# Kernel tuning notes

Hardware: AMD Instinct MI355X
Metric: run time of the kernel (lower is better)

Reference implementation:

```python
import jax, jax.numpy as jnp
import numpy as np

B, V, D = 8, 2048, 3
CL1_F, CL1_K = 64, 6
CL2_F, CL2_K = 128, 5
F1, F2 = 512, 256


def _uniform(k, shape, fin, fout):
    s = np.sqrt(2.0 / (fin + fout)).astype(np.float32)
    return jax.random.uniform(k, shape, jnp.float32, -s, s)


def setup_inputs() -> dict:
    key = jax.random.key(0)
    ks = jax.random.split(key, 8)
    x = jax.random.normal(ks[0], (B, D, V), jnp.float32)
    # dense stand-in for the scaled graph Laplacian; scaled so spectral radius < 1
    L = jax.random.normal(ks[1], (B, V, V), jnp.float32) * (0.5 / np.sqrt(V))
    L = 0.5 * (L + L.transpose(0, 2, 1))  # symmetric like a real Laplacian
    return {
        "x": x,
        "L": L,
        "cl1_w": _uniform(ks[2], (CL1_F, D * CL1_K), CL1_K, CL1_F),
        "cl1_b": jnp.zeros((CL1_F,), jnp.float32),
        "cl2_w": _uniform(ks[3], (CL2_F, CL2_K * CL1_F), CL2_K * CL1_F, CL2_F),
        "cl2_b": jnp.zeros((CL2_F,), jnp.float32),
        "fc1_w": _uniform(ks[4], (F1, CL2_F), CL2_F, F1),
        "fc1_b": jnp.zeros((F1,), jnp.float32),
        "fc2_w": _uniform(ks[5], (F2, F1), F1, F2),
        "fc2_b": jnp.zeros((F2,), jnp.float32),
    }


def _cheby_conv(x, L, W, b, K):
    # x: [B, V, Fin], L: [B, V, V] -> [B, V, Fout]
    x0 = x
    xs = [x0]
    if K > 1:
        x1 = jnp.einsum('bvu,buf->bvf', L, x0)
        xs.append(x1)
    for _ in range(2, K):
        x2 = 2.0 * jnp.einsum('bvu,buf->bvf', L, x1) - x0
        xs.append(x2)
        x0, x1 = x1, x2
    # torch ordering: feature index = fin * K + k  -> stack K on last axis
    xk = jnp.stack(xs, axis=-1)                 # [B, V, Fin, K]
    xk = xk.reshape(xk.shape[0], xk.shape[1], -1)  # [B, V, Fin*K]
    return xk @ W.T + b


def reference(x, L, cl1_w, cl1_b, cl2_w, cl2_b, fc1_w, fc1_b, fc2_w, fc2_b):
    xp = x.transpose(0, 2, 1)                    # [B, V, D]
    y = jax.nn.relu(_cheby_conv(xp, L, cl1_w, cl1_b, CL1_K))
    y = jax.nn.relu(_cheby_conv(y, L, cl2_w, cl2_b, CL2_K))
    y = jax.nn.relu(y @ fc1_w.T + fc1_b)
    y = jax.nn.relu(y @ fc2_w.T + fc2_b)
    return y                                     # [B, V, F2]
```

## Files before the change

### kernel.cpp

```cpp
#include <hip/hip_runtime.h>

#define B_ 8
#define V_ 2048
#define D_ 3
#define M_ (B_*V_)

typedef __attribute__((ext_vector_type(8))) short short8;
typedef __attribute__((ext_vector_type(4))) float f32x4;

__device__ inline void async_copy16(const void* g, void* lds) {
  __builtin_amdgcn_global_load_lds(
      (const __attribute__((address_space(1))) unsigned int*)g,
      (__attribute__((address_space(3))) unsigned int*)lds, 16, 0, 0);
}

__device__ inline void split_bf16(float v, short& hi, short& lo) {
  unsigned u  = __float_as_uint(v);
  unsigned hb = u & 0xFFFF0000u;
  float d = v - __uint_as_float(hb);
  hi = (short)(hb >> 16);
  lo = (short)(__float_as_uint(d) >> 16);
}

__global__ __launch_bounds__(256) void k_zero(float4* __restrict__ p, int n4) {
  int i = blockIdx.x * 256 + threadIdx.x;
  if (i < n4) p[i] = float4{0.f, 0.f, 0.f, 0.f};
}

__global__ __launch_bounds__(256) void k_split_pad(const float* __restrict__ src,
    short* __restrict__ dh, short* __restrict__ dl, int N, int K, int Kpad) {
  int idx = blockIdx.x * 256 + threadIdx.x;
  if (idx >= N * Kpad) return;
  int n = idx / Kpad, k = idx - n * Kpad;
  float v = (k < K) ? src[(size_t)n*K + k] : 0.f;
  short hi, lo; split_bf16(v, hi, lo);
  dh[idx] = hi; dl[idx] = lo;
}

__global__ __launch_bounds__(256) void k_transpose(const float* __restrict__ x,
    float* __restrict__ x0, short* __restrict__ XKh, short* __restrict__ XKl) {
  int i = blockIdx.x * 256 + threadIdx.x;
  if (i >= B_*V_*D_) return;
  int f = i % D_;
  int v = (i / D_) % V_;
  int b = i / (D_*V_);
  float val = x[((size_t)b*D_ + f)*V_ + v];
  x0[i] = val;
  short hi, lo; split_bf16(val, hi, lo);
  size_t o = ((size_t)b*V_ + v)*64 + f*6;
  XKh[o] = hi; XKl[o] = lo;
}

__global__ __launch_bounds__(256) void k_cheby1(const float* __restrict__ L,
    const float* __restrict__ xc, const float* __restrict__ xp,
    float* __restrict__ xn, short* __restrict__ XKh, short* __restrict__ XKl,
    float alpha, float beta, int kidx) {
  __shared__ float sx[3][V_];
  int b  = blockIdx.x >> 6;
  int r0 = (blockIdx.x & 63) * 32;
  const float* xcb = xc + (size_t)b*V_*D_;
  for (int i = threadIdx.x; i < V_*D_; i += 256) {
    int u = i / 3, f = i - u*3;
    sx[f][u] = xcb[i];
  }
  __syncthreads();
  int w = threadIdx.x >> 6, lane = threadIdx.x & 63;
  const float4* X0 = (const float4*)sx[0];
  const float4* X1 = (const float4*)sx[1];
  const float4* X2 = (const float4*)sx[2];
  for (int pass = 0; pass < 4; pass++) {
    int rA = r0 + pass*8 + w*2;
    int rB = rA + 1;
    const float4* LA = (const float4*)(L + ((size_t)b*V_ + rA)*V_);
    const float4* LB = (const float4*)(L + ((size_t)b*V_ + rB)*V_);
    float a0=0.f,a1=0.f,a2=0.f,b0=0.f,b1=0.f,b2=0.f;
    #pragma unroll
    for (int it = 0; it < 8; it++) {
      int u4 = it*64 + lane;
      float4 la = LA[u4], lb = LB[u4];
      float4 x0 = X0[u4], x1 = X1[u4], x2 = X2[u4];
      a0 = fmaf(la.x,x0.x,fmaf(la.y,x0.y,fmaf(la.z,x0.z,fmaf(la.w,x0.w,a0))));
      a1 = fmaf(la.x,x1.x,fmaf(la.y,x1.y,fmaf(la.z,x1.z,fmaf(la.w,x1.w,a1))));
      a2 = fmaf(la.x,x2.x,fmaf(la.y,x2.y,fmaf(la.z,x2.z,fmaf(la.w,x2.w,a2))));
      b0 = fmaf(lb.x,x0.x,fmaf(lb.y,x0.y,fmaf(lb.z,x0.z,fmaf(lb.w,x0.w,b0))));
      b1 = fmaf(lb.x,x1.x,fmaf(lb.y,x1.y,fmaf(lb.z,x1.z,fmaf(lb.w,x1.w,b1))));
      b2 = fmaf(lb.x,x2.x,fmaf(lb.y,x2.y,fmaf(lb.z,x2.z,fmaf(lb.w,x2.w,b2))));
    }
    #pragma unroll
    for (int off = 32; off > 0; off >>= 1) {
      a0 += __shfl_down(a0, off); a1 += __shfl_down(a1, off);
      a2 += __shfl_down(a2, off); b0 += __shfl_down(b0, off);
      b1 += __shfl_down(b1, off); b2 += __shfl_down(b2, off);
    }
    if (lane == 0) {
      float vA[3] = {alpha*a0, alpha*a1, alpha*a2};
      float vB[3] = {alpha*b0, alpha*b1, alpha*b2};
      size_t baseA = ((size_t)b*V_ + rA)*3;
      size_t baseB = ((size_t)b*V_ + rB)*3;
      if (beta != 0.f) {
        #pragma unroll
        for (int f = 0; f < 3; f++) {
          vA[f] -= beta * xp[baseA + f];
          vB[f] -= beta * xp[baseB + f];
        }
      }
      #pragma unroll
      for (int f = 0; f < 3; f++) {
        xn[baseA + f] = vA[f];
        xn[baseB + f] = vB[f];
        short hi, lo;
        split_bf16(vA[f], hi, lo);
        size_t oA = ((size_t)b*V_ + rA)*64 + f*6 + kidx;
        XKh[oA] = hi; XKl[oA] = lo;
        split_bf16(vB[f], hi, lo);
        size_t oB = ((size_t)b*V_ + rB)*64 + f*6 + kidx;
        XKh[oB] = hi; XKl[oB] = lo;
      }
    }
  }
}

__global__ __launch_bounds__(256) void k_split_t(const float* __restrict__ Z,
    short* __restrict__ Th, short* __restrict__ Tl) {
  __shared__ float t[64][65];
  int b  = blockIdx.x >> 5;
  int r0 = (blockIdx.x & 31) * 64;
  const float* Zb = Z + ((size_t)b*V_ + r0)*64;
  #pragma unroll 4
  for (int i = 0; i < 16; i++) {
    int idx = i*256 + threadIdx.x;
    int r = idx >> 6, n = idx & 63;
    t[r][n] = Zb[(size_t)r*64 + n];
  }
  __syncthreads();
  #pragma unroll 4
  for (int i = 0; i < 16; i++) {
    int idx = i*256 + threadIdx.x;
    int n = idx >> 6, r = idx & 63;
    short hi, lo; split_bf16(t[r][n], hi, lo);
    size_t o = ((size_t)b*64 + n)*V_ + r0 + r;
    Th[o] = hi; Tl[o] = lo;
  }
}

__global__ __launch_bounds__(256) void k_cheby2_mfma(const float* __restrict__ L,
    const short* __restrict__ Zth, const short* __restrict__ Ztl,
    const float* __restrict__ Zp,
    float* __restrict__ Zn, short* __restrict__ ZKh, short* __restrict__ ZKl,
    short* __restrict__ Znth, short* __restrict__ Zntl,
    float alpha, float beta, int kidx) {
  __shared__ float sA[32*64];
  __shared__ short sBh[64*64];
  __shared__ short sBl[64*64];

  int b  = blockIdx.x >> 6;
  int r0 = (blockIdx.x & 63) * 32;
  const float* Lb   = L   + (size_t)b*V_*V_;
  const short* Zthb = Zth + (size_t)b*64*V_;
  const short* Ztlb = Ztl + (size_t)b*64*V_;

  int tid  = threadIdx.x;
  int w    = tid >> 6;
  int lane = tid & 63;
  int lm   = lane & 15;
  int quad = lane >> 4;
  int h     = (w & 1) * 16;
  int cbase = (w >> 1) * 32;

  const f32x4*  sAv  = (const f32x4*)sA;
  const short8* sBhv = (const short8*)sBh;
  const short8* sBlv = (const short8*)sBl;

  f32x4 acc0 = {0.f,0.f,0.f,0.f};
  f32x4 acc1 = {0.f,0.f,0.f,0.f};

  for (int s = 0; s < V_/64; s++) {
    int k0 = s * 64;
    if (s) __syncthreads();
    #pragma unroll
    for (int t = 0; t < 2; t++) {
      int f = t*256 + tid;
      int r = f >> 4, cc = f & 15;
      int c = cc ^ (r & 15);
      async_copy16(Lb + (size_t)(r0 + r)*V_ + k0 + c*4, &sA[f*4]);
    }
    #pragma unroll
    for (int t = 0; t < 2; t++) {
      int f = t*256 + tid;
      int n = f >> 3, cc = f & 7;
      int c = cc ^ (n & 7);
      async_copy16(Zthb + (size_t)n*V_ + k0 + c*8, &sBh[f*8]);
      async_copy16(Ztlb + (size_t)n*V_ + k0 + c*8, &sBl[f*8]);
    }
    __syncthreads();

    #pragma unroll
    for (int ks = 0; ks < 2; ks++) {
      int koff = ks * 32;
      int r = h + lm;
      int c0 = (koff >> 2) + 2*quad;
      f32x4 a0 = sAv[r*16 + (c0 ^ (r & 15))];
      f32x4 a1 = sAv[r*16 + ((c0 + 1) ^ (r & 15))];
      float av[8] = {a0.x, a0.y, a0.z, a0.w, a1.x, a1.y, a1.z, a1.w};
      short8 ah, al;
      #pragma unroll
      for (int j = 0; j < 8; j++) {
        short hi, lo; split_bf16(av[j], hi, lo);
        ah[j] = hi; al[j] = lo;
      }
      int cb = (koff >> 3) + quad;
      {
        int n = cbase + lm;
        short8 bh = sBhv[n*8 + (cb ^ (n & 7))];
        short8 bl = sBlv[n*8 + (cb ^ (n & 7))];
        acc0 = __builtin_amdgcn_mfma_f32_16x16x32_bf16(ah, bh, acc0, 0, 0, 0);
        acc0 = __builtin_amdgcn_mfma_f32_16x16x32_bf16(ah, bl, acc0, 0, 0, 0);
        acc0 = __builtin_amdgcn_mfma_f32_16x16x32_bf16(al, bh, acc0, 0, 0, 0);
      }
      {
        int n = cbase + 16 + lm;
        short8 bh = sBhv[n*8 + (cb ^ (n & 7))];
        short8 bl = sBlv[n*8 + (cb ^ (n & 7))];
        acc1 = __builtin_amdgcn_mfma_f32_16x16x32_bf16(ah, bh, acc1, 0, 0, 0);
        acc1 = __builtin_amdgcn_mfma_f32_16x16x32_bf16(ah, bl, acc1, 0, 0, 0);
        acc1 = __builtin_amdgcn_mfma_f32_16x16x32_bf16(al, bh, acc1, 0, 0, 0);
      }
    }
  }

  #pragma unroll
  for (int ct = 0; ct < 2; ct++) {
    f32x4 a = ct ? acc1 : acc0;
    int n = cbase + ct*16 + lm;
    #pragma unroll
    for (int i = 0; i < 4; i++) {
      int r = r0 + h + quad*4 + i;
      size_t rowb = (size_t)b*V_ + r;
      float v = alpha * a[i];
      if (beta != 0.f) v -= beta * Zp[rowb*64 + n];
      Zn[rowb*64 + n] = v;
      short hi, lo; split_bf16(v, hi, lo);
      size_t ok = rowb*320 + (size_t)n*5 + kidx;
      ZKh[ok] = hi; ZKl[ok] = lo;
      size_t o = ((size_t)b*64 + n)*V_ + r;
      Znth[o] = hi; Zntl[o] = lo;
    }
  }
}

__global__ __launch_bounds__(256) void k_gemm_bf16(
    const short* __restrict__ Ah, const short* __restrict__ Al,
    const short* __restrict__ Wh, const short* __restrict__ Wl,
    const float* __restrict__ bias, int N, int K,
    float* __restrict__ Cf, short* __restrict__ Ch, short* __restrict__ Cl,
    short* __restrict__ Ph, short* __restrict__ Pl,
    int packMul, int packStride) {
  __shared__ short sAh[64*64], sAl[64*64], sWh[64*64], sWl[64*64];
  int bm = blockIdx.x & 255;
  int bn = blockIdx.x >> 8;
  int row0 = bm * 64, col0 = bn * 64;
  int tid = threadIdx.x, w = tid >> 6, lane = tid & 63;
  int lm = lane & 15, quad = lane >> 4;
  int wm = (w & 1) * 32, wn = (w >> 1) * 32;

  const short8* vAh = (const short8*)sAh;
  const short8* vAl = (const short8*)sAl;
  const short8* vWh = (const short8*)sWh;
  const short8* vWl = (const short8*)sWl;

  f32x4 acc[2][2] = {{{0.f,0.f,0.f,0.f},{0.f,0.f,0.f,0.f}},
                     {{0.f,0.f,0.f,0.f},{0.f,0.f,0.f,0.f}}};

  for (int k0 = 0; k0 < K; k0 += 64) {
    if (k0) __syncthreads();
    #pragma unroll
    for (int t = 0; t < 2; t++) {
      int f = t*256 + tid;
      int r = f >> 3, p = f & 7;
      int c = p ^ (r & 7);
      size_t goA = (size_t)(row0 + r)*K + k0 + c*8;
      size_t goW = (size_t)(col0 + r)*K + k0 + c*8;
      async_copy16(Ah + goA, &sAh[f*8]);
      async_copy16(Al + goA, &sAl[f*8]);
      async_copy16(Wh + goW, &sWh[f*8]);
      async_copy16(Wl + goW, &sWl[f*8]);
    }
    __syncthreads();

    #pragma unroll
    for (int ks = 0; ks < 2; ks++) {
      int kc = ks*4 + quad;
      short8 a_h[2], a_l[2], b_h[2], b_l[2];
      #pragma unroll
      for (int i = 0; i < 2; i++) {
        int m = wm + i*16 + lm;
        a_h[i] = vAh[m*8 + (kc ^ (m & 7))];
        a_l[i] = vAl[m*8 + (kc ^ (m & 7))];
      }
      #pragma unroll
      for (int j = 0; j < 2; j++) {
        int n = wn + j*16 + lm;
        b_h[j] = vWh[n*8 + (kc ^ (n & 7))];
        b_l[j] = vWl[n*8 + (kc ^ (n & 7))];
      }
      #pragma unroll
      for (int i = 0; i < 2; i++)
        #pragma unroll
        for (int j = 0; j < 2; j++) {
          acc[i][j] = __builtin_amdgcn_mfma_f32_16x16x32_bf16(a_h[i], b_h[j], acc[i][j], 0, 0, 0);
          acc[i][j] = __builtin_amdgcn_mfma_f32_16x16x32_bf16(a_h[i], b_l[j], acc[i][j], 0, 0, 0);
          acc[i][j] = __builtin_amdgcn_mfma_f32_16x16x32_bf16(a_l[i], b_h[j], acc[i][j], 0, 0, 0);
        }
    }
  }

  #pragma unroll
  for (int i = 0; i < 2; i++)
    #pragma unroll
    for (int j = 0; j < 2; j++) {
      int col = col0 + wn + j*16 + lm;
      float bj = bias[col];
      #pragma unroll
      for (int g = 0; g < 4; g++) {
        int row = row0 + wm + i*16 + quad*4 + g;
        float v = acc[i][j][g] + bj;
        v = v > 0.f ? v : 0.f;
        if (Cf) Cf[(size_t)row*N + col] = v;
        if (Ch) {
          short hi, lo; split_bf16(v, hi, lo);
          Ch[(size_t)row*N + col] = hi;
          Cl[(size_t)row*N + col] = lo;
        }
        if (Ph) {
          short hi, lo; split_bf16(v, hi, lo);
          size_t o = (size_t)row*packStride + (size_t)col*packMul;
          Ph[o] = hi; Pl[o] = lo;
        }
      }
    }
}

extern "C" void kernel_launch(void* const* d_in, const int* in_sizes, int n_in,
                              void* d_out, int out_size, void* d_ws, size_t ws_size,
                              hipStream_t stream) {
  const float* x   = (const float*)d_in[0];
  const float* L   = (const float*)d_in[1];
  const float* w1  = (const float*)d_in[2];
  const float* b1  = (const float*)d_in[3];
  const float* w2  = (const float*)d_in[4];
  const float* b2  = (const float*)d_in[5];
  const float* fw1 = (const float*)d_in[6];
  const float* fb1 = (const float*)d_in[7];
  const float* fw2 = (const float*)d_in[8];
  const float* fb2 = (const float*)d_in[9];
  float* out = (float*)d_out;

  float* p  = (float*)d_ws;
  float* xa = p;  p += (size_t)B_*V_*D_;
  float* xb = p;  p += (size_t)B_*V_*D_;
  float* xc = p;  p += (size_t)B_*V_*D_;
  float* y1 = p;  p += (size_t)M_*64;
  float* zb = p;  p += (size_t)M_*64;
  float* zc = p;  p += (size_t)M_*64;
  short* sp = (short*)p;
  short* ZKh = sp;  sp += (size_t)M_*320;
  short* ZKl = sp;  sp += (size_t)M_*320;
  short* y2h = sp;  sp += (size_t)M_*128;
  short* y2l = sp;  sp += (size_t)M_*128;
  short* h1h = sp;  sp += (size_t)M_*512;
  short* h1l = sp;  sp += (size_t)M_*512;
  short* ZtAh = sp; sp += (size_t)M_*64;
  short* ZtAl = sp; sp += (size_t)M_*64;
  short* ZtBh = sp; sp += (size_t)M_*64;
  short* ZtBl = sp; sp += (size_t)M_*64;
  short* w1h = sp;  sp += 64*64;
  short* w1l = sp;  sp += 64*64;
  short* w2h = sp;  sp += 128*320;
  short* w2l = sp;  sp += 128*320;
  short* fw1h = sp; sp += 512*128;
  short* fw1l = sp; sp += 512*128;
  short* fw2h = sp; sp += 256*512;
  short* fw2l = sp; sp += 256*512;
  short* XKh = h1h;
  short* XKl = h1h + (size_t)M_*64;

  dim3 blk(256);

  k_zero<<<1024, blk, 0, stream>>>((float4*)XKh, (M_*128) / 8);

  k_split_pad<<<(64*64+255)/256,   blk, 0, stream>>>(w1,  w1h,  w1l,  64, 18, 64);
  k_split_pad<<<(128*320+255)/256, blk, 0, stream>>>(w2,  w2h,  w2l,  128, 320, 320);
  k_split_pad<<<(512*128+255)/256, blk, 0, stream>>>(fw1, fw1h, fw1l, 512, 128, 128);
  k_split_pad<<<(256*512+255)/256, blk, 0, stream>>>(fw2, fw2h, fw2l, 256, 512, 512);

  k_transpose<<<(B_*V_*D_ + 255)/256, blk, 0, stream>>>(x, xa, XKh, XKl);

  k_cheby1<<<512, blk, 0, stream>>>(L, xa, xa, xb, XKh, XKl, 1.f, 0.f, 1);
  k_cheby1<<<512, blk, 0, stream>>>(L, xb, xa, xc, XKh, XKl, 2.f, 1.f, 2);
  k_cheby1<<<512, blk, 0, stream>>>(L, xc, xb, xa, XKh, XKl, 2.f, 1.f, 3);
  k_cheby1<<<512, blk, 0, stream>>>(L, xa, xc, xb, XKh, XKl, 2.f, 1.f, 4);
  k_cheby1<<<512, blk, 0, stream>>>(L, xb, xa, xc, XKh, XKl, 2.f, 1.f, 5);

  k_gemm_bf16<<<256, blk, 0, stream>>>(XKh, XKl, w1h, w1l, b1, 64, 64,
                                       y1, nullptr, nullptr, ZKh, ZKl, 5, 320);

  k_split_t<<<256, blk, 0, stream>>>(y1, ZtAh, ZtAl);

  k_cheby2_mfma<<<512, blk, 0, stream>>>(L, ZtAh, ZtAl, y1, zb, ZKh, ZKl,
                                         ZtBh, ZtBl, 1.f, 0.f, 1);
  k_cheby2_mfma<<<512, blk, 0, stream>>>(L, ZtBh, ZtBl, y1, zc, ZKh, ZKl,
                                         ZtAh, ZtAl, 2.f, 1.f, 2);
  k_cheby2_mfma<<<512, blk, 0, stream>>>(L, ZtAh, ZtAl, zb, y1, ZKh, ZKl,
                                         ZtBh, ZtBl, 2.f, 1.f, 3);
  k_cheby2_mfma<<<512, blk, 0, stream>>>(L, ZtBh, ZtBl, zc, zb, ZKh, ZKl,
                                         ZtAh, ZtAl, 2.f, 1.f, 4);

  k_gemm_bf16<<<512, blk, 0, stream>>>(ZKh, ZKl, w2h, w2l, b2, 128, 320,
                                       nullptr, y2h, y2l, nullptr, nullptr, 0, 0);
  k_gemm_bf16<<<2048, blk, 0, stream>>>(y2h, y2l, fw1h, fw1l, fb1, 512, 128,
                                        nullptr, h1h, h1l, nullptr, nullptr, 0, 0);
  k_gemm_bf16<<<1024, blk, 0, stream>>>(h1h, h1l, fw2h, fw2l, fb2, 256, 512,
                                        out, nullptr, nullptr, nullptr, nullptr, 0, 0);
}
```

Measured before the change: 594.7 us.

## Fuse prep kernels, shrink Chebyshev row tiles, fold transpose into first GEMM

Merges the zero-fill, weight split/pad and input transpose launches into one prep kernel. It also fuses the y1 transpose-split into the first GEMM epilogue, which drops the separate k_split_t pass. The Chebyshev kernels now use smaller row tiles (8 rows for cheby1, 16 for cheby2), which quadruples or doubles the grid to spread the L-bandwidth-bound work over more CUs. In exchange, each block reloads the x/Z operand more often: cheby1 restages all of x into LDS per block, and more blocks now read the full Zt slices.

New measurement: 540.1 us. 9.2% less time.

```diff
diff --git a/kernel.cpp b/kernel.cpp
--- a/kernel.cpp
+++ b/kernel.cpp
@@ -22,33 +22,43 @@
   lo = (short)(__float_as_uint(d) >> 16);
 }
 
-__global__ __launch_bounds__(256) void k_zero(float4* __restrict__ p, int n4) {
+__global__ __launch_bounds__(256) void k_prep(
+    const float* __restrict__ x,
+    const float* __restrict__ w1, const float* __restrict__ w2,
+    const float* __restrict__ fw1, const float* __restrict__ fw2,
+    float* __restrict__ xa,
+    short* __restrict__ XKh, short* __restrict__ XKl,
+    short* __restrict__ w1h, short* __restrict__ w1l,
+    short* __restrict__ w2h, short* __restrict__ w2l,
+    short* __restrict__ fw1h, short* __restrict__ fw1l,
+    short* __restrict__ fw2h, short* __restrict__ fw2l) {
   int i = blockIdx.x * 256 + threadIdx.x;
-  if (i < n4) p[i] = float4{0.f, 0.f, 0.f, 0.f};
-}
-
-__global__ __launch_bounds__(256) void k_split_pad(const float* __restrict__ src,
-    short* __restrict__ dh, short* __restrict__ dl, int N, int K, int Kpad) {
-  int idx = blockIdx.x * 256 + threadIdx.x;
-  if (idx >= N * Kpad) return;
-  int n = idx / Kpad, k = idx - n * Kpad;
-  float v = (k < K) ? src[(size_t)n*K + k] : 0.f;
-  short hi, lo; split_bf16(v, hi, lo);
-  dh[idx] = hi; dl[idx] = lo;
-}
-
-__global__ __launch_bounds__(256) void k_transpose(const float* __restrict__ x,
-    float* __restrict__ x0, short* __restrict__ XKh, short* __restrict__ XKl) {
-  int i = blockIdx.x * 256 + threadIdx.x;
-  if (i >= B_*V_*D_) return;
-  int f = i % D_;
-  int v = (i / D_) % V_;
-  int b = i / (D_*V_);
-  float val = x[((size_t)b*D_ + f)*V_ + v];
-  x0[i] = val;
-  short hi, lo; split_bf16(val, hi, lo);
-  size_t o = ((size_t)b*V_ + v)*64 + f*6;
-  XKh[o] = hi; XKl[o] = lo;
+  short hi, lo;
+  if (i < M_*64) {
+    int r = i >> 6, s = i & 63;
+    float val = 0.f;
+    if (s == 0 || s == 6 || s == 12) {
+      int f = s / 6;
+      int b = r >> 11, v = r & (V_-1);
+      val = x[((size_t)b*D_ + f)*V_ + v];
+      xa[(size_t)r*3 + f] = val;
+    }
+    split_bf16(val, hi, lo);
+    XKh[i] = hi; XKl[i] = lo;
+    return;
+  }
+  i -= M_*64;
+  if (i < 4096) {
+    int n = i >> 6, k = i & 63;
+    float v = (k < 18) ? w1[n*18 + k] : 0.f;
+    split_bf16(v, hi, lo); w1h[i] = hi; w1l[i] = lo; return;
+  }
+  i -= 4096;
+  if (i < 40960) { split_bf16(w2[i],  hi, lo); w2h[i]=hi;  w2l[i]=lo;  return; }
+  i -= 40960;
+  if (i < 65536) { split_bf16(fw1[i], hi, lo); fw1h[i]=hi; fw1l[i]=lo; return; }
+  i -= 65536;
+  if (i < 131072){ split_bf16(fw2[i], hi, lo); fw2h[i]=hi; fw2l[i]=lo; return; }
 }
 
 __global__ __launch_bounds__(256) void k_cheby1(const float* __restrict__ L,
@@ -56,8 +66,8 @@
     float* __restrict__ xn, short* __restrict__ XKh, short* __restrict__ XKl,
     float alpha, float beta, int kidx) {
   __shared__ float sx[3][V_];
-  int b  = blockIdx.x >> 6;
-  int r0 = (blockIdx.x & 63) * 32;
+  int b  = blockIdx.x >> 8;
+  int r0 = (blockIdx.x & 255) * 8;
   const float* xcb = xc + (size_t)b*V_*D_;
   for (int i = threadIdx.x; i < V_*D_; i += 256) {
     int u = i / 3, f = i - u*3;
@@ -68,78 +78,53 @@
   const float4* X0 = (const float4*)sx[0];
   const float4* X1 = (const float4*)sx[1];
   const float4* X2 = (const float4*)sx[2];
-  for (int pass = 0; pass < 4; pass++) {
-    int rA = r0 + pass*8 + w*2;
-    int rB = rA + 1;
-    const float4* LA = (const float4*)(L + ((size_t)b*V_ + rA)*V_);
-    const float4* LB = (const float4*)(L + ((size_t)b*V_ + rB)*V_);
-    float a0=0.f,a1=0.f,a2=0.f,b0=0.f,b1=0.f,b2=0.f;
-    #pragma unroll
-    for (int it = 0; it < 8; it++) {
-      int u4 = it*64 + lane;
-      float4 la = LA[u4], lb = LB[u4];
-      float4 x0 = X0[u4], x1 = X1[u4], x2 = X2[u4];
-      a0 = fmaf(la.x,x0.x,fmaf(la.y,x0.y,fmaf(la.z,x0.z,fmaf(la.w,x0.w,a0))));
-      a1 = fmaf(la.x,x1.x,fmaf(la.y,x1.y,fmaf(la.z,x1.z,fmaf(la.w,x1.w,a1))));
-      a2 = fmaf(la.x,x2.x,fmaf(la.y,x2.y,fmaf(la.z,x2.z,fmaf(la.w,x2.w,a2))));
-      b0 = fmaf(lb.x,x0.x,fmaf(lb.y,x0.y,fmaf(lb.z,x0.z,fmaf(lb.w,x0.w,b0))));
-      b1 = fmaf(lb.x,x1.x,fmaf(lb.y,x1.y,fmaf(lb.z,x1.z,fmaf(lb.w,x1.w,b1))));
-      b2 = fmaf(lb.x,x2.x,fmaf(lb.y,x2.y,fmaf(lb.z,x2.z,fmaf(lb.w,x2.w,b2))));
-    }
-    #pragma unroll
-    for (int off = 32; off > 0; off >>= 1) {
-      a0 += __shfl_down(a0, off); a1 += __shfl_down(a1, off);
-      a2 += __shfl_down(a2, off); b0 += __shfl_down(b0, off);
-      b1 += __shfl_down(b1, off); b2 += __shfl_down(b2, off);
-    }
-    if (lane == 0) {
-      float vA[3] = {alpha*a0, alpha*a1, alpha*a2};
-      float vB[3] = {alpha*b0, alpha*b1, alpha*b2};
-      size_t baseA = ((size_t)b*V_ + rA)*3;
-      size_t baseB = ((size_t)b*V_ + rB)*3;
-      if (beta != 0.f) {
-        #pragma unroll
-        for (int f = 0; f < 3; f++) {
-          vA[f] -= beta * xp[baseA + f];
-          vB[f] -= beta * xp[baseB + f];
-        }
+  int rA = r0 + w*2;
+  int rB = rA + 1;
+  const float4* LA = (const float4*)(L + ((size_t)b*V_ + rA)*V_);
+  const float4* LB = (const float4*)(L + ((size_t)b*V_ + rB)*V_);
+  float a0=0.f,a1=0.f,a2=0.f,b0=0.f,b1=0.f,b2=0.f;
+  #pragma unroll
+  for (int it = 0; it < 8; it++) {
+    int u4 = it*64 + lane;
+    float4 la = LA[u4], lb = LB[u4];
+    float4 x0 = X0[u4], x1 = X1[u4], x2 = X2[u4];
+    a0 = fmaf(la.x,x0.x,fmaf(la.y,x0.y,fmaf(la.z,x0.z,fmaf(la.w,x0.w,a0))));
+    a1 = fmaf(la.x,x1.x,fmaf(la.y,x1.y,fmaf(la.z,x1.z,fmaf(la.w,x1.w,a1))));
+    a2 = fmaf(la.x,x2.x,fmaf(la.y,x2.y,fmaf(la.z,x2.z,fmaf(la.w,x2.w,a2))));
+    b0 = fmaf(lb.x,x0.x,fmaf(lb.y,x0.y,fmaf(lb.z,x0.z,fmaf(lb.w,x0.w,b0))));
+    b1 = fmaf(lb.x,x1.x,fmaf(lb.y,x1.y,fmaf(lb.z,x1.z,fmaf(lb.w,x1.w,b1))));
+    b2 = fmaf(lb.x,x2.x,fmaf(lb.y,x2.y,fmaf(lb.z,x2.z,fmaf(lb.w,x2.w,b2))));
+  }
+  #pragma unroll
+  for (int off = 32; off > 0; off >>= 1) {
+    a0 += __shfl_down(a0, off); a1 += __shfl_down(a1, off);
+    a2 += __shfl_down(a2, off); b0 += __shfl_down(b0, off);
+    b1 += __shfl_down(b1, off); b2 += __shfl_down(b2, off);
+  }
+  if (lane == 0) {
+    float vA[3] = {alpha*a0, alpha*a1, alpha*a2};
+    float vB[3] = {alpha*b0, alpha*b1, alpha*b2};
+    size_t baseA = ((size_t)b*V_ + rA)*3;
+    size_t baseB = ((size_t)b*V_ + rB)*3;
+    if (beta != 0.f) {
+      #pragma unroll
+      for (int f = 0; f < 3; f++) {
+        vA[f] -= beta * xp[baseA + f];
+        vB[f] -= beta * xp[baseB + f];
       }
-      #pragma unroll
-      for (int f = 0; f < 3; f++) {
-        xn[baseA + f] = vA[f];
-        xn[baseB + f] = vB[f];
-        short hi, lo;
-        split_bf16(vA[f], hi, lo);
-        size_t oA = ((size_t)b*V_ + rA)*64 + f*6 + kidx;
-        XKh[oA] = hi; XKl[oA] = lo;
-        split_bf16(vB[f], hi, lo);
-        size_t oB = ((size_t)b*V_ + rB)*64 + f*6 + kidx;
-        XKh[oB] = hi; XKl[oB] = lo;
-      }
-    }
-  }
-}
-
-__global__ __launch_bounds__(256) void k_split_t(const float* __restrict__ Z,
-    short* __restrict__ Th, short* __restrict__ Tl) {
-  __shared__ float t[64][65];
-  int b  = blockIdx.x >> 5;
-  int r0 = (blockIdx.x & 31) * 64;
-  const float* Zb = Z + ((size_t)b*V_ + r0)*64;
-  #pragma unroll 4
-  for (int i = 0; i < 16; i++) {
-    int idx = i*256 + threadIdx.x;
-    int r = idx >> 6, n = idx & 63;
-    t[r][n] = Zb[(size_t)r*64 + n];
-  }
-  __syncthreads();
-  #pragma unroll 4
-  for (int i = 0; i < 16; i++) {
-    int idx = i*256 + threadIdx.x;
-    int n = idx >> 6, r = idx & 63;
-    short hi, lo; split_bf16(t[r][n], hi, lo);
-    size_t o = ((size_t)b*64 + n)*V_ + r0 + r;
-    Th[o] = hi; Tl[o] = lo;
+    }
+    #pragma unroll
+    for (int f = 0; f < 3; f++) {
+      xn[baseA + f] = vA[f];
+      xn[baseB + f] = vB[f];
+      short hi, lo;
+      split_bf16(vA[f], hi, lo);
+      size_t oA = ((size_t)b*V_ + rA)*64 + f*6 + kidx;
+      XKh[oA] = hi; XKl[oA] = lo;
+      split_bf16(vB[f], hi, lo);
+      size_t oB = ((size_t)b*V_ + rB)*64 + f*6 + kidx;
+      XKh[oB] = hi; XKl[oB] = lo;
+    }
   }
 }
 
@@ -149,12 +134,12 @@
     float* __restrict__ Zn, short* __restrict__ ZKh, short* __restrict__ ZKl,
     short* __restrict__ Znth, short* __restrict__ Zntl,
     float alpha, float beta, int kidx) {
-  __shared__ float sA[32*64];
+  __shared__ float sA[16*64];
   __shared__ short sBh[64*64];
   __shared__ short sBl[64*64];
 
-  int b  = blockIdx.x >> 6;
-  int r0 = (blockIdx.x & 63) * 32;
+  int b  = blockIdx.x >> 7;
+  int r0 = (blockIdx.x & 127) * 16;
   const float* Lb   = L   + (size_t)b*V_*V_;
   const short* Zthb = Zth + (size_t)b*64*V_;
   const short* Ztlb = Ztl + (size_t)b*64*V_;
@@ -164,24 +149,21 @@
   int lane = tid & 63;
   int lm   = lane & 15;
   int quad = lane >> 4;
-  int h     = (w & 1) * 16;
-  int cbase = (w >> 1) * 32;
+  int cbase = w * 16;
 
   const f32x4*  sAv  = (const f32x4*)sA;
   const short8* sBhv = (const short8*)sBh;
   const short8* sBlv = (const short8*)sBl;
 
-  f32x4 acc0 = {0.f,0.f,0.f,0.f};
-  f32x4 acc1 = {0.f,0.f,0.f,0.f};
+  f32x4 acc = {0.f,0.f,0.f,0.f};
 
   for (int s = 0; s < V_/64; s++) {
     int k0 = s * 64;
     if (s) __syncthreads();
-    #pragma unroll
-    for (int t = 0; t < 2; t++) {
-      int f = t*256 + tid;
+    {
+      int f = tid;
       int r = f >> 4, cc = f & 15;
-      int c = cc ^ (r & 15);
+      int c = cc ^ r;
       async_copy16(Lb + (size_t)(r0 + r)*V_ + k0 + c*4, &sA[f*4]);
     }
     #pragma unroll
@@ -197,10 +179,10 @@
     #pragma unroll
     for (int ks = 0; ks < 2; ks++) {
       int koff = ks * 32;
-      int r = h + lm;
+      int r = lm;
       int c0 = (koff >> 2) + 2*quad;
-      f32x4 a0 = sAv[r*16 + (c0 ^ (r & 15))];
-      f32x4 a1 = sAv[r*16 + ((c0 + 1) ^ (r & 15))];
+      f32x4 a0 = sAv[r*16 + (c0 ^ r)];
+      f32x4 a1 = sAv[r*16 + ((c0 + 1) ^ r)];
       float av[8] = {a0.x, a0.y, a0.z, a0.w, a1.x, a1.y, a1.z, a1.w};
       short8 ah, al;
       #pragma unroll
@@ -209,56 +191,39 @@
         ah[j] = hi; al[j] = lo;
       }
       int cb = (koff >> 3) + quad;
-      {
-        int n = cbase + lm;
-        short8 bh = sBhv[n*8 + (cb ^ (n & 7))];
-        short8 bl = sBlv[n*8 + (cb ^ (n & 7))];
-        acc0 = __builtin_amdgcn_mfma_f32_16x16x32_bf16(ah, bh, acc0, 0, 0, 0);
-        acc0 = __builtin_amdgcn_mfma_f32_16x16x32_bf16(ah, bl, acc0, 0, 0, 0);
-        acc0 = __builtin_amdgcn_mfma_f32_16x16x32_bf16(al, bh, acc0, 0, 0, 0);
-      }
-      {
-        int n = cbase + 16 + lm;
-        short8 bh = sBhv[n*8 + (cb ^ (n & 7))];
-        short8 bl = sBlv[n*8 + (cb ^ (n & 7))];
-        acc1 = __builtin_amdgcn_mfma_f32_16x16x32_bf16(ah, bh, acc1, 0, 0, 0);
-        acc1 = __builtin_amdgcn_mfma_f32_16x16x32_bf16(ah, bl, acc1, 0, 0, 0);
-        acc1 = __builtin_amdgcn_mfma_f32_16x16x32_bf16(al, bh, acc1, 0, 0, 0);
-      }
-    }
-  }
-
+      int n = cbase + lm;
+      short8 bh = sBhv[n*8 + (cb ^ (n & 7))];
+      short8 bl = sBlv[n*8 + (cb ^ (n & 7))];
+      acc = __builtin_amdgcn_mfma_f32_16x16x32_bf16(ah, bh, acc, 0, 0, 0);
+      acc = __builtin_amdgcn_mfma_f32_16x16x32_bf16(ah, bl, acc, 0, 0, 0);
+      acc = __builtin_amdgcn_mfma_f32_16x16x32_bf16(al, bh, acc, 0, 0, 0);
+    }
+  }
+
+  int n = cbase + lm;
   #pragma unroll
-  for (int ct = 0; ct < 2; ct++) {
-    f32x4 a = ct ? acc1 : acc0;
-    int n = cbase + ct*16 + lm;
-    #pragma unroll
-    for (int i = 0; i < 4; i++) {
-      int r = r0 + h + quad*4 + i;
-      size_t rowb = (size_t)b*V_ + r;
-      float v = alpha * a[i];
-      if (beta != 0.f) v -= beta * Zp[rowb*64 + n];
-      Zn[rowb*64 + n] = v;
-      short hi, lo; split_bf16(v, hi, lo);
-      size_t ok = rowb*320 + (size_t)n*5 + kidx;
-      ZKh[ok] = hi; ZKl[ok] = lo;
-      size_t o = ((size_t)b*64 + n)*V_ + r;
-      Znth[o] = hi; Zntl[o] = lo;
-    }
-  }
-}
-
-__global__ __launch_bounds__(256) void k_gemm_bf16(
+  for (int i = 0; i < 4; i++) {
+    int r = r0 + quad*4 + i;
+    size_t rowb = (size_t)b*V_ + r;
+    float v = alpha * acc[i];
+    if (beta != 0.f) v -= beta * Zp[rowb*64 + n];
+    Zn[rowb*64 + n] = v;
+    short hi, lo; split_bf16(v, hi, lo);
+    size_t ok = rowb*320 + (size_t)n*5 + kidx;
+    ZKh[ok] = hi; ZKl[ok] = lo;
+    size_t o = ((size_t)b*64 + n)*V_ + r;
+    Znth[o] = hi; Zntl[o] = lo;
+  }
+}
+
+__device__ __forceinline__ void gemm_tile(
     const short* __restrict__ Ah, const short* __restrict__ Al,
     const short* __restrict__ Wh, const short* __restrict__ Wl,
-    const float* __restrict__ bias, int N, int K,
+    const float* __restrict__ bias, int N, int K, int row0, int col0,
+    short* sAh, short* sAl, short* sWh, short* sWl,
     float* __restrict__ Cf, short* __restrict__ Ch, short* __restrict__ Cl,
-    short* __restrict__ Ph, short* __restrict__ Pl,
-    int packMul, int packStride) {
-  __shared__ short sAh[64*64], sAl[64*64], sWh[64*64], sWl[64*64];
-  int bm = blockIdx.x & 255;
-  int bn = blockIdx.x >> 8;
-  int row0 = bm * 64, col0 = bn * 64;
+    short* __restrict__ Ph, short* __restrict__ Pl, int packMul, int packStride,
+    short* __restrict__ Th, short* __restrict__ Tl) {
   int tid = threadIdx.x, w = tid >> 6, lane = tid & 63;
   int lm = lane & 15, quad = lane >> 4;
   int wm = (w & 1) * 32, wn = (w >> 1) * 32;
@@ -326,18 +291,48 @@
         float v = acc[i][j][g] + bj;
         v = v > 0.f ? v : 0.f;
         if (Cf) Cf[(size_t)row*N + col] = v;
+        short hi, lo;
+        if (Ch || Ph || Th) split_bf16(v, hi, lo);
         if (Ch) {
-          short hi, lo; split_bf16(v, hi, lo);
           Ch[(size_t)row*N + col] = hi;
           Cl[(size_t)row*N + col] = lo;
         }
         if (Ph) {
-          short hi, lo; split_bf16(v, hi, lo);
           size_t o = (size_t)row*packStride + (size_t)col*packMul;
           Ph[o] = hi; Pl[o] = lo;
         }
+        if (Th) {
+          int bb = row >> 11, vv = row & (V_-1);
+          size_t o = ((size_t)bb*64 + col)*V_ + vv;
+          Th[o] = hi; Tl[o] = lo;
+        }
       }
     }
+}
+
+__global__ __launch_bounds__(256) void k_gemm_y1(
+    const short* __restrict__ XKh, const short* __restrict__ XKl,
+    const short* __restrict__ w1h, const short* __restrict__ w1l,
+    const float* __restrict__ b1, float* __restrict__ y1,
+    short* __restrict__ ZKh, short* __restrict__ ZKl,
+    short* __restrict__ Th, short* __restrict__ Tl) {
+  __shared__ short sAh[64*64], sAl[64*64], sWh[64*64], sWl[64*64];
+  gemm_tile(XKh, XKl, w1h, w1l, b1, 64, 64, blockIdx.x*64, 0,
+            sAh, sAl, sWh, sWl,
+            y1, nullptr, nullptr, ZKh, ZKl, 5, 320, Th, Tl);
+}
+
+__global__ __launch_bounds__(256) void k_gemm_bf16(
+    const short* __restrict__ Ah, const short* __restrict__ Al,
+    const short* __restrict__ Wh, const short* __restrict__ Wl,
+    const float* __restrict__ bias, int N, int K,
+    float* __restrict__ Cf, short* __restrict__ Ch, short* __restrict__ Cl) {
+  __shared__ short sAh[64*64], sAl[64*64], sWh[64*64], sWl[64*64];
+  int bm = blockIdx.x & 255;
+  int bn = blockIdx.x >> 8;
+  gemm_tile(Ah, Al, Wh, Wl, bias, N, K, bm*64, bn*64,
+            sAh, sAl, sWh, sWl,
+            Cf, Ch, Cl, nullptr, nullptr, 0, 0, nullptr, nullptr);
 }
 
 extern "C" void kernel_launch(void* const* d_in, const int* in_sizes, int n_in,
@@ -384,41 +379,32 @@
   short* XKh = h1h;
   short* XKl = h1h + (size_t)M_*64;
 
-  dim3 blk(256);
-
-  k_zero<<<1024, blk, 0, stream>>>((float4*)XKh, (M_*128) / 8);
-
-  k_split_pad<<<(64*64+255)/256,   blk, 0, stream>>>(w1,  w1h,  w1l,  64, 18, 64);
-  k_split_pad<<<(128*320+255)/256, blk, 0, stream>>>(w2,  w2h,  w2l,  128, 320, 320);
-  k_split_pad<<<(512*128+255)/256, blk, 0, stream>>>(fw1, fw1h, fw1l, 512, 128, 128);
-  k_split_pad<<<(256*512+255)/256, blk, 0, stream>>>(fw2, fw2h, fw2l, 256, 512, 512);
-
-  k_transpose<<<(B_*V_*D_ + 255)/256, blk, 0, stream>>>(x, xa, XKh, XKl);
-
-  k_cheby1<<<512, blk, 0, stream>>>(L, xa, xa, xb, XKh, XKl, 1.f, 0.f, 1);
-  k_cheby1<<<512, blk, 0, stream>>>(L, xb, xa, xc, XKh, XKl, 2.f, 1.f, 2);
-  k_cheby1<<<512, blk, 0, stream>>>(L, xc, xb, xa, XKh, XKl, 2.f, 1.f, 3);
-  k_cheby1<<<512, blk, 0, stream>>>(L, xa, xc, xb, XKh, XKl, 2.f, 1.f, 4);
-  k_cheby1<<<512, blk, 0, stream>>>(L, xb, xa, xc, XKh, XKl, 2.f, 1.f, 5);
-
-  k_gemm_bf16<<<256, blk, 0, stream>>>(XKh, XKl, w1h, w1l, b1, 64, 64,
-                                       y1, nullptr, nullptr, ZKh, ZKl, 5, 320);
-
-  k_split_t<<<256, blk, 0, stream>>>(y1, ZtAh, ZtAl);
-
-  k_cheby2_mfma<<<512, blk, 0, stream>>>(L, ZtAh, ZtAl, y1, zb, ZKh, ZKl,
-                                         ZtBh, ZtBl, 1.f, 0.f, 1);
-  k_cheby2_mfma<<<512, blk, 0, stream>>>(L, ZtBh, ZtBl, y1, zc, ZKh, ZKl,
-                                         ZtAh, ZtAl, 2.f, 1.f, 2);
-  k_cheby2_mfma<<<512, blk, 0, stream>>>(L, ZtAh, ZtAl, zb, y1, ZKh, ZKl,
-                                         ZtBh, ZtBl, 2.f, 1.f, 3);
-  k_cheby2_mfma<<<512, blk, 0, stream>>>(L, ZtBh, ZtBl, zc, zb, ZKh, ZKl,
-                                         ZtAh, ZtAl, 2.f, 1.f, 4);
-
-  k_gemm_bf16<<<512, blk, 0, stream>>>(ZKh, ZKl, w2h, w2l, b2, 128, 320,
-                                       nullptr, y2h, y2l, nullptr, nullptr, 0, 0);
-  k_gemm_bf16<<<2048, blk, 0, stream>>>(y2h, y2l, fw1h, fw1l, fb1, 512, 128,
-                                        nullptr, h1h, h1l, nullptr, nullptr, 0, 0);
-  k_gemm_bf16<<<1024, blk, 0, stream>>>(h1h, h1l, fw2h, fw2l, fb2, 256, 512,
-                                        out, nullptr, nullptr, nullptr, nullptr, 0, 0);
-}
+  k_prep<<<5040, 256, 0, stream>>>(x, w1, w2, fw1, fw2, xa,
+                                   XKh, XKl, w1h, w1l, w2h, w2l,
+                                   fw1h, fw1l, fw2h, fw2l);
+
+  k_cheby1<<<2048, 256, 0, stream>>>(L, xa, xa, xb, XKh, XKl, 1.f, 0.f, 1);
+  k_cheby1<<<2048, 256, 0, stream>>>(L, xb, xa, xc, XKh, XKl, 2.f, 1.f, 2);
+  k_cheby1<<<2048, 256, 0, stream>>>(L, xc, xb, xa, XKh, XKl, 2.f, 1.f, 3);
+  k_cheby1<<<2048, 256, 0, stream>>>(L, xa, xc, xb, XKh, XKl, 2.f, 1.f, 4);
+  k_cheby1<<<2048, 256, 0, stream>>>(L, xb, xa, xc, XKh, XKl, 2.f, 1.f, 5);
+
+  k_gemm_y1<<<256, 256, 0, stream>>>(XKh, XKl, w1h, w1l, b1,
+                                     y1, ZKh, ZKl, ZtAh, ZtAl);
+
+  k_cheby2_mfma<<<1024, 256, 0, stream>>>(L, ZtAh, ZtAl, y1, zb, ZKh, ZKl,
+                                          ZtBh, ZtBl, 1.f, 0.f, 1);
+  k_cheby2_mfma<<<1024, 256, 0, stream>>>(L, ZtBh, ZtBl, y1, zc, ZKh, ZKl,
+                                          ZtAh, ZtAl, 2.f, 1.f, 2);
+  k_cheby2_mfma<<<1024, 256, 0, stream>>>(L, ZtAh, ZtAl, zb, y1, ZKh, ZKl,
+                                          ZtBh, ZtBl, 2.f, 1.f, 3);
+  k_cheby2_mfma<<<1024, 256, 0, stream>>>(L, ZtBh, ZtBl, zc, zb, ZKh, ZKl,
+                                          ZtAh, ZtAl, 2.f, 1.f, 4);
+
+  k_gemm_bf16<<<512, 256, 0, stream>>>(ZKh, ZKl, w2h, w2l, b2, 128, 320,
+                                       nullptr, y2h, y2l);
+  k_gemm_bf16<<<2048, 256, 0, stream>>>(y2h, y2l, fw1h, fw1l, fb1, 512, 128,
+                                        nullptr, h1h, h1l);
+  k_gemm_bf16<<<1024, 256, 0, stream>>>(h1h, h1l, fw2h, fw2l, fb2, 256, 512,
+                                        out, nullptr, nullptr);
+}
```
